# Performance work log

Measured on AMD Instinct MI355X. Metric: run time of the kernel, lower is better.

The kernel has to match this reference:

```python
import jax, jax.numpy as jnp
import numpy as np
from jax import lax

NC = 8  # num_classes
NUM_ITERS = 2


def _resize_bilinear_ac(x, out_h, out_w):
    """Bilinear resize with align_corners=True, x: (N, C, H, W)."""
    N, C, H, W = x.shape

    def coords(n_out, n_in):
        if n_out == 1:
            return jnp.zeros((1,), jnp.float32)
        return jnp.linspace(0.0, float(n_in - 1), n_out, dtype=jnp.float32)

    ys = coords(out_h, H)
    xs = coords(out_w, W)
    y0 = jnp.floor(ys).astype(jnp.int32)
    y1 = jnp.minimum(y0 + 1, H - 1)
    wy = (ys - y0.astype(jnp.float32)).astype(x.dtype)
    x0 = jnp.floor(xs).astype(jnp.int32)
    x1 = jnp.minimum(x0 + 1, W - 1)
    wx = (xs - x0.astype(jnp.float32)).astype(x.dtype)

    r0 = x[:, :, y0, :]
    r1 = x[:, :, y1, :]
    r = r0 * (1.0 - wy)[None, None, :, None] + r1 * wy[None, None, :, None]
    c0 = r[:, :, :, x0]
    c1 = r[:, :, :, x1]
    return c0 * (1.0 - wx)[None, None, None, :] + c1 * wx[None, None, None, :]


def _conv2d(x, w, groups=1):
    k = w.shape[-1]
    pad = k // 2
    return lax.conv_general_dilated(
        x, w, window_strides=(1, 1), padding=[(pad, pad), (pad, pad)],
        dimension_numbers=('NCHW', 'OIHW', 'NCHW'), feature_group_count=groups)


def _mean_field_update(unary, guidance, spatial_w, bilateral_w, compat_w):
    Q = jax.nn.softmax(unary, axis=1)
    cw = compat_w[:, :, 0, 0]  # (O, I)
    for _ in range(NUM_ITERS):
        spatial_msg = _conv2d(Q, spatial_w, groups=NC)          # depthwise 3x3
        bilateral_in = jnp.concatenate([Q, guidance], axis=1)   # (N, NC+6, H, W)
        bilateral_msg = _conv2d(bilateral_in, bilateral_w)      # 3x3 dense
        message = spatial_msg + bilateral_msg
        message = jnp.einsum('nchw,oc->nohw', message, cw)      # 1x1 compat conv
        Q = jax.nn.softmax(unary - message, axis=1)
    return Q


def setup_inputs() -> dict:
    key = jax.random.key(0)
    ks = jax.random.split(key, 16)
    inp = {
        'logits': jax.random.normal(ks[0], (8, NC, 512, 512), jnp.float32),
        'image': jax.random.uniform(ks[1], (8, 3, 512, 512), jnp.float32),
        'skip0': jax.random.normal(ks[2], (8, 64, 256, 256), jnp.float32),
        'skip1': jax.random.normal(ks[3], (8, 128, 128, 128), jnp.float32),
        'skip2': jax.random.normal(ks[4], (8, 256, 64, 64), jnp.float32),
        'skip3': jax.random.normal(ks[5], (8, 512, 32, 32), jnp.float32),
        'spatial_w': jax.random.normal(ks[6], (NC, 1, 3, 3), jnp.float32) * 0.1,
        'bilateral_w': jax.random.normal(ks[7], (NC, NC + 6, 3, 3), jnp.float32) * 0.1,
        # compat_conv is initialized to -I (zeros then -= eye) in the module
        'compat_w': (-jnp.eye(NC, dtype=jnp.float32)).reshape(NC, NC, 1, 1),
        'skip_w0': jax.random.normal(ks[8], (3, 64, 1, 1), jnp.float32) * 0.05,
        'skip_b0': jnp.zeros((3,), jnp.float32),
        'skip_w1': jax.random.normal(ks[9], (3, 128, 1, 1), jnp.float32) * 0.05,
        'skip_b1': jnp.zeros((3,), jnp.float32),
        'skip_w2': jax.random.normal(ks[10], (3, 256, 1, 1), jnp.float32) * 0.05,
        'skip_b2': jnp.zeros((3,), jnp.float32),
        'skip_w3': jax.random.normal(ks[11], (3, 512, 1, 1), jnp.float32) * 0.05,
        'skip_b3': jnp.zeros((3,), jnp.float32),
    }
    return inp


def reference(logits, image, skip0, skip1, skip2, skip3,
              spatial_w, bilateral_w, compat_w,
              skip_w0, skip_b0, skip_w1, skip_b1,
              skip_w2, skip_b2, skip_w3, skip_b3):
    H, W = logits.shape[2], logits.shape[3]

    # fuse_skip_features: 1x1 project each skip to 3ch, upsample, average
    skips = [skip0, skip1, skip2, skip3]
    ws = [skip_w0, skip_w1, skip_w2, skip_w3]
    bs = [skip_b0, skip_b1, skip_b2, skip_b3]
    fused = jnp.zeros((logits.shape[0], 3, H, W), logits.dtype)
    for feat, w, b in zip(skips, ws, bs):
        p = jnp.einsum('nchw,oc->nohw', feat, w[:, :, 0, 0]) + b[None, :, None, None]
        fused = fused + _resize_bilinear_ac(p, H, W)
    fused = fused / len(skips)

    guidance = jnp.concatenate([image, fused], axis=1)  # (N, 6, H, W)

    Q_full = _mean_field_update(logits, guidance, spatial_w, bilateral_w, compat_w)

    logits_down = _resize_bilinear_ac(logits, H // 2, W // 2)
    guidance_down = _resize_bilinear_ac(guidance, H // 2, W // 2)
    Q_down = _mean_field_update(logits_down, guidance_down, spatial_w, bilateral_w, compat_w)
    Q_down_up = _resize_bilinear_ac(Q_down, H, W)

    return (Q_full + Q_down_up) / 2.0
```

## Files before the change

kernel.cpp:

```cpp
#include <hip/hip_runtime.h>
#include <hip/hip_fp16.h>
#include <math.h>

#define NB 8
#define NCLS 8
#define NGU 6
#define NBI 14
#define HF 512
#define WF 512
#define HH 256
#define WH 256

#define TOX 32
#define TOY 16
#define SX 36
#define SY 20
#define SPX (SY * SX)
#define R1W 36
#define R1N (18 * 36)
#define R1T 41
#define R2T 32
#define PLANE (SPX * 8)
#define PSTR (PLANE + 32)
#define TILEH (16 + PSTR + PLANE + 16)

typedef _Float16 f16x8 __attribute__((ext_vector_type(8)));
typedef float f32x4 __attribute__((ext_vector_type(4)));

static __device__ __forceinline__ void ac_prep(int o, float scale, int insz,
                                               int& i0, int& i1, float& f) {
    float s = (float)o * scale;
    int ii = (int)floorf(s);
    if (ii > insz - 1) ii = insz - 1;
    if (ii < 0) ii = 0;
    i0 = ii;
    i1 = (ii + 1 < insz) ? (ii + 1) : (insz - 1);
    f = s - (float)ii;
}

static __device__ __forceinline__ void dma16(const _Float16* g, _Float16* l) {
    __builtin_amdgcn_global_load_lds(
        (const __attribute__((address_space(1))) void*)g,
        (__attribute__((address_space(3))) void*)l, 16, 0, 0);
}

__global__ void k_fill3(float* __restrict__ p1, float* __restrict__ p2,
                        float* __restrict__ p3, const float* __restrict__ b1,
                        const float* __restrict__ b2, const float* __restrict__ b3) {
    int i = blockIdx.x * blockDim.x + threadIdx.x;
    if (i < NB * 3 * 16384) { p1[i] = b1[(i / 16384) % 3]; return; }
    i -= NB * 3 * 16384;
    if (i < NB * 3 * 4096) { p2[i] = b2[(i / 4096) % 3]; return; }
    i -= NB * 3 * 4096;
    if (i < NB * 3 * 1024) p3[i] = b3[(i / 1024) % 3];
}

template <int VEC, bool DIRECT>
__global__ void k_skip_proj(const float* __restrict__ feat, const float* __restrict__ w,
                            const float* __restrict__ bias, float* __restrict__ out,
                            int C, int HW, int nch) {
    __shared__ float sw[3 * 512];
    for (int i = threadIdx.x; i < 3 * C; i += blockDim.x) sw[i] = w[i];
    __syncthreads();
    const int HWv = HW / VEC;
    int total = NB * HWv * nch;
    for (int idx = blockIdx.x * blockDim.x + threadIdx.x; idx < total;
         idx += gridDim.x * blockDim.x) {
        int hv = idx % HWv;
        int t = idx / HWv;
        int ch = t % nch;
        int n = t / nch;
        int c0 = ch * 64;
        const float* fp = feat + ((size_t)n * C + c0) * HW + (size_t)hv * VEC;
        float a[3][VEC];
        #pragma unroll
        for (int o = 0; o < 3; ++o)
            #pragma unroll
            for (int k = 0; k < VEC; ++k) a[o][k] = 0.f;
        #pragma unroll 4
        for (int c = 0; c < 64; ++c) {
            float v[VEC];
            if constexpr (VEC == 4) {
                float4 t4 = *reinterpret_cast<const float4*>(fp + (size_t)c * HW);
                v[0] = t4.x; v[1] = t4.y; v[2] = t4.z; v[3] = t4.w;
            } else if constexpr (VEC == 2) {
                float2 t2 = *reinterpret_cast<const float2*>(fp + (size_t)c * HW);
                v[0] = t2.x; v[1] = t2.y;
            } else {
                v[0] = fp[(size_t)c * HW];
            }
            #pragma unroll
            for (int o = 0; o < 3; ++o) {
                const float wv = sw[o * C + c0 + c];
                #pragma unroll
                for (int k = 0; k < VEC; ++k) a[o][k] = fmaf(wv, v[k], a[o][k]);
            }
        }
        float* op = out + (size_t)n * 3 * HW + (size_t)hv * VEC;
        #pragma unroll
        for (int o = 0; o < 3; ++o) {
            #pragma unroll
            for (int k = 0; k < VEC; ++k) {
                if (DIRECT)
                    op[(size_t)o * HW + k] = bias[o] + a[o][k];
                else
                    atomicAdd(&op[(size_t)o * HW + k], a[o][k]);
            }
        }
    }
}

__global__ void k_prep_full(const float* __restrict__ logits, const float* __restrict__ image,
                            const float* __restrict__ p0, const float* __restrict__ p1,
                            const float* __restrict__ p2, const float* __restrict__ p3,
                            _Float16* __restrict__ Gh, _Float16* __restrict__ Q0h) {
    const int HW = HF * WF;
    int t = blockIdx.x * blockDim.x + threadIdx.x;
    if (t >= NB * HW / 2) return;
    int idx = t * 2;
    int n = idx / HW, r = idx - n * HW;
    int y = r / WF, x = r - y * WF;

    const float* ps[4] = {p0, p1, p2, p3};
    const int ss[4] = {256, 128, 64, 32};
    float f[2][3] = {{0.f, 0.f, 0.f}, {0.f, 0.f, 0.f}};
    #pragma unroll
    for (int l = 0; l < 4; ++l) {
        int s = ss[l];
        float scale = (float)(s - 1) / 511.0f;
        int y0, y1;
        float fy;
        ac_prep(y, scale, s, y0, y1, fy);
        const float* pb = ps[l] + (size_t)n * 3 * s * s;
        #pragma unroll
        for (int k = 0; k < 2; ++k) {
            int x0, x1;
            float fx;
            ac_prep(x + k, scale, s, x0, x1, fx);
            #pragma unroll
            for (int o = 0; o < 3; ++o) {
                const float* pp = pb + (size_t)o * s * s;
                float v00 = pp[y0 * s + x0], v01 = pp[y0 * s + x1];
                float v10 = pp[y1 * s + x0], v11 = pp[y1 * s + x1];
                float r0 = v00 * (1.f - fy) + v10 * fy;
                float r1 = v01 * (1.f - fy) + v11 * fy;
                f[k][o] += r0 * (1.f - fx) + r1 * fx;
            }
        }
    }
    const float* ip = image + (size_t)n * 3 * HW + r;
    float2 img[3];
    #pragma unroll
    for (int o = 0; o < 3; ++o) img[o] = *reinterpret_cast<const float2*>(&ip[(size_t)o * HW]);
    const float* up = logits + (size_t)n * NCLS * HW + r;
    float2 u[8];
    #pragma unroll
    for (int o = 0; o < 8; ++o) u[o] = *reinterpret_cast<const float2*>(&up[(size_t)o * HW]);

    f16x8 gv[2], qv[2];
    #pragma unroll
    for (int k = 0; k < 2; ++k) {
        gv[k][0] = (_Float16)(k ? img[0].y : img[0].x);
        gv[k][1] = (_Float16)(k ? img[1].y : img[1].x);
        gv[k][2] = (_Float16)(k ? img[2].y : img[2].x);
        gv[k][3] = (_Float16)(f[k][0] * 0.25f);
        gv[k][4] = (_Float16)(f[k][1] * 0.25f);
        gv[k][5] = (_Float16)(f[k][2] * 0.25f);
        gv[k][6] = (_Float16)0.f;
        gv[k][7] = (_Float16)0.f;
        float e[8];
        float s = 0.f;
        #pragma unroll
        for (int o = 0; o < 8; ++o) { e[o] = __expf(k ? u[o].y : u[o].x); s += e[o]; }
        float inv = 1.f / s;
        #pragma unroll
        for (int o = 0; o < 8; ++o) qv[k][o] = (_Float16)(e[o] * inv);
    }
    *(f16x8*)(Gh + (size_t)idx * 8) = gv[0];
    *(f16x8*)(Gh + (size_t)idx * 8 + 8) = gv[1];
    *(f16x8*)(Q0h + (size_t)idx * 8) = qv[0];
    *(f16x8*)(Q0h + (size_t)idx * 8 + 8) = qv[1];
}

__global__ void k_prep_wf(const float* __restrict__ wsp, const float* __restrict__ wbil,
                          const float* __restrict__ cw, _Float16* __restrict__ wf) {
    __shared__ float sW2[NBI * 72];
    int tid = threadIdx.x;
    if (tid < NBI * 72) {
        int o = tid & 7;
        int t = (tid >> 3) % 9;
        int ci = tid / 72;
        float s = 0.f;
        for (int c = 0; c < NCLS; ++c)
            s += cw[o * NCLS + c] * wbil[((size_t)c * NBI + ci) * 9 + t];
        if (ci < NCLS) s += cw[o * NCLS + ci] * wsp[ci * 9 + t];
        sW2[tid] = s;
    }
    __syncthreads();
    if (tid < 5 * 64) {
        int l = tid & 63;
        int col = l & 15, kg = l >> 4;
        #pragma unroll
        for (int e = 0; e < 8; ++e) {
            int k = (tid >> 6) * 32 + kg * 8 + e;
            int tap = k >> 4, ci = k & 15;
            float v = (tap < 9 && ci < 14 && col < 8) ? sW2[ci * 72 + tap * 8 + col] : 0.f;
            wf[tid * 8 + e] = (_Float16)v;
        }
    }
}

template <bool DOWN, bool UPFOLD>
__global__ __launch_bounds__(256, 4) void k_mf_mfma(
    const float* __restrict__ unary, const _Float16* __restrict__ Q0h,
    const _Float16* __restrict__ Gh, const _Float16* __restrict__ Qd,
    void* __restrict__ QoutV, const _Float16* __restrict__ wfragG,
    int H, int W, int Hs, int Ws) {
    __shared__ __align__(16) _Float16 s_t[TILEH];
    __shared__ __align__(16) _Float16 s_msg[R1N * 8];
    _Float16* tb0 = s_t + 16;
    _Float16* tb1 = s_t + 16 + PSTR;

    const int tid = threadIdx.x;
    const int lane = tid & 63;
    const int wv = tid >> 6;
    const int n = blockIdx.z;
    const int gx0 = blockIdx.x * TOX;
    const int gy0 = blockIdx.y * TOY;
    const int HW = H * W;
    const int HWs = Hs * Ws;

    f16x8 wf[5];
    #pragma unroll
    for (int j = 0; j < 5; ++j)
        wf[j] = *(const f16x8*)(wfragG + (j * 64 + lane) * 8);

    if (tid < 16) s_t[tid] = (_Float16)0.f;
    else if (tid < 48) s_t[5760 + tid] = (_Float16)0.f;
    else if (tid < 64) s_t[11520 + tid] = (_Float16)0.f;

    const bool interior = !DOWN && gx0 >= 2 && (gx0 + TOX + 2) <= W &&
                          gy0 >= 2 && (gy0 + TOY + 2) <= H;

    if (!DOWN && interior) {
        const size_t nb = (size_t)n * HW;
        for (int c = wv; c < 12; c += 4) {
            int px = c * 64 + lane;
            int yy = px / SX, xx = px - yy * SX;
            size_t goff = (nb + (size_t)(gy0 + yy - 2) * W + (gx0 + xx - 2)) * 8;
            if (px < SPX) {
                dma16(Q0h + goff, tb0 + (size_t)c * 64 * 8);
                dma16(Gh + goff, tb1 + (size_t)c * 64 * 8);
            }
        }
    } else {
        const float syc = DOWN ? (float)(Hs - 1) / (float)(H - 1) : 1.f;
        const float sxc = DOWN ? (float)(Ws - 1) / (float)(W - 1) : 1.f;
        for (int i = tid; i < SPX; i += 256) {
            int yy = i / SX, xx = i - yy * SX;
            int gy = gy0 + yy - 2, gx = gx0 + xx - 2;
            f16x8 qv, gv;
            #pragma unroll
            for (int o = 0; o < 8; ++o) { qv[o] = (_Float16)0.f; gv[o] = (_Float16)0.f; }
            if ((unsigned)gy < (unsigned)H && (unsigned)gx < (unsigned)W) {
                if (DOWN) {
                    int y0, y1, x0, x1;
                    float fy, fx;
                    ac_prep(gy, syc, Hs, y0, y1, fy);
                    ac_prep(gx, sxc, Ws, x0, x1, fx);
                    const float w00 = (1.f - fy) * (1.f - fx), w01 = (1.f - fy) * fx;
                    const float w10 = fy * (1.f - fx), w11 = fy * fx;
                    const size_t o00 = (size_t)y0 * Ws + x0, o01 = (size_t)y0 * Ws + x1;
                    const size_t o10 = (size_t)y1 * Ws + x0, o11 = (size_t)y1 * Ws + x1;
                    const float* ubase = unary + (size_t)n * NCLS * HWs;
                    float e[8];
                    float s = 0.f;
                    #pragma unroll
                    for (int o = 0; o < 8; ++o) {
                        const float* up = ubase + (size_t)o * HWs;
                        float u = w00 * up[o00] + w01 * up[o01] + w10 * up[o10] + w11 * up[o11];
                        e[o] = __expf(u);
                        s += e[o];
                    }
                    float inv = 1.f / s;
                    #pragma unroll
                    for (int o = 0; o < 8; ++o) qv[o] = (_Float16)(e[o] * inv);
                    const size_t gb = (size_t)n * HWs;
                    f16x8 ga = *(const f16x8*)(Gh + (gb + o00) * 8);
                    f16x8 gb2 = *(const f16x8*)(Gh + (gb + o01) * 8);
                    f16x8 gc = *(const f16x8*)(Gh + (gb + o10) * 8);
                    f16x8 gd = *(const f16x8*)(Gh + (gb + o11) * 8);
                    #pragma unroll
                    for (int c = 0; c < 8; ++c) {
                        float g = w00 * (float)ga[c] + w01 * (float)gb2[c] +
                                  w10 * (float)gc[c] + w11 * (float)gd[c];
                        gv[c] = (_Float16)g;
                    }
                } else {
                    const size_t off = ((size_t)n * HW + (size_t)gy * W + gx) * 8;
                    qv = *(const f16x8*)(Q0h + off);
                    gv = *(const f16x8*)(Gh + off);
                }
            }
            *(f16x8*)(tb0 + i * 8) = qv;
            *(f16x8*)(tb1 + i * 8) = gv;
        }
    }
    __syncthreads();

    for (int t = wv; t < R1T; t += 4) {
        int pb = t * 16;
        int p = pb + (lane & 15);
        if (p > R1N - 1) p = R1N - 1;
        int qy = p / R1W;
        int yy = 1 + qy, xx = p - qy * R1W;
        int kg = lane >> 4;
        f32x4 acc = {0.f, 0.f, 0.f, 0.f};
        #pragma unroll
        for (int j = 0; j < 5; ++j) {
            int tap = 2 * j + (kg >> 1);
            if (tap > 8) tap = 8;
            int dy = tap / 3 - 1, dx = tap - (tap / 3) * 3 - 1;
            int idx = (yy + dy) * SX + (xx + dx);
            f16x8 af = *(const f16x8*)(tb0 + (kg & 1) * PSTR + idx * 8);
            acc = __builtin_amdgcn_mfma_f32_16x16x32_f16(af, wf[j], acc, 0, 0, 0);
        }
        int ch = lane & 15;
        if (ch < 8) {
            int pxb = pb + (lane >> 4) * 4;
            #pragma unroll
            for (int r = 0; r < 4; ++r) {
                int px = pxb + r;
                if (px < R1N) s_msg[px * 8 + ch] = (_Float16)acc[r];
            }
        }
    }
    __syncthreads();

    for (int i = tid; i < R1N; i += 256) {
        int qy = i / R1W;
        int yy = 1 + qy, xx = i - qy * R1W;
        int gy = gy0 + yy - 2, gx = gx0 + xx - 2;
        if (interior || ((unsigned)gy < (unsigned)H && (unsigned)gx < (unsigned)W)) {
            f16x8 m = *(const f16x8*)(s_msg + i * 8);
            f16x8 q0 = *(const f16x8*)(tb0 + (i + SX) * 8);
            float e[8];
            float s = 0.f;
            #pragma unroll
            for (int o = 0; o < 8; ++o) {
                e[o] = (float)q0[o] * __expf(-(float)m[o]);
                s += e[o];
            }
            float inv = 1.f / s;
            f16x8 q1;
            #pragma unroll
            for (int o = 0; o < 8; ++o) q1[o] = (_Float16)(e[o] * inv);
            *(f16x8*)(tb0 + (i + SX) * 8) = q1;
        }
    }
    f16x8 m1r[2];
    #pragma unroll
    for (int u2 = 0; u2 < 2; ++u2) {
        int i = tid + 256 * u2;
        int oy = i >> 5, ox = i & 31;
        int r1 = (1 + oy) * R1W + (2 + ox);
        m1r[u2] = *(const f16x8*)(s_msg + r1 * 8);
    }
    __syncthreads();

    for (int t = wv; t < R2T; t += 4) {
        int pb = t * 16;
        int p = pb + (lane & 15);
        int yy = 2 + (p >> 5), xx = 2 + (p & 31);
        int kg = lane >> 4;
        f32x4 acc = {0.f, 0.f, 0.f, 0.f};
        #pragma unroll
        for (int j = 0; j < 5; ++j) {
            int tap = 2 * j + (kg >> 1);
            if (tap > 8) tap = 8;
            int dy = tap / 3 - 1, dx = tap - (tap / 3) * 3 - 1;
            int idx = (yy + dy) * SX + (xx + dx);
            f16x8 af = *(const f16x8*)(tb0 + (kg & 1) * PSTR + idx * 8);
            acc = __builtin_amdgcn_mfma_f32_16x16x32_f16(af, wf[j], acc, 0, 0, 0);
        }
        int ch = lane & 15;
        if (ch < 8) {
            int pxb = pb + (lane >> 4) * 4;
            #pragma unroll
            for (int r = 0; r < 4; ++r) s_msg[(pxb + r) * 8 + ch] = (_Float16)acc[r];
        }
    }
    __syncthreads();

    #pragma unroll
    for (int u2 = 0; u2 < 2; ++u2) {
        int i = tid + 256 * u2;
        int oy = i >> 5, ox = i & 31;
        int gy = gy0 + oy, gx = gx0 + ox;
        f16x8 m2 = *(const f16x8*)(s_msg + i * 8);
        f16x8 q1 = *(const f16x8*)(tb0 + ((2 + oy) * SX + (2 + ox)) * 8);
        float e[8];
        float s = 0.f;
        #pragma unroll
        for (int o = 0; o < 8; ++o) {
            e[o] = (float)q1[o] * __expf((float)m1r[u2][o] - (float)m2[o]);
            s += e[o];
        }
        float inv = 1.f / s;
        if (UPFOLD) {
            float* qp = (float*)QoutV + (size_t)n * NCLS * HW + (size_t)gy * W + gx;
            int y0, y1, x0, x1;
            float fy, fx;
            ac_prep(gy, 255.f / 511.f, HH, y0, y1, fy);
            ac_prep(gx, 255.f / 511.f, WH, x0, x1, fx);
            const float w00 = (1.f - fy) * (1.f - fx), w01 = (1.f - fy) * fx;
            const float w10 = fy * (1.f - fx), w11 = fy * fx;
            const size_t qb = (size_t)n * (HH * WH);
            f16x8 qa = *(const f16x8*)(Qd + (qb + (size_t)y0 * WH + x0) * 8);
            f16x8 qbv = *(const f16x8*)(Qd + (qb + (size_t)y0 * WH + x1) * 8);
            f16x8 qc = *(const f16x8*)(Qd + (qb + (size_t)y1 * WH + x0) * 8);
            f16x8 qdv = *(const f16x8*)(Qd + (qb + (size_t)y1 * WH + x1) * 8);
            #pragma unroll
            for (int o = 0; o < 8; ++o) {
                float v = w00 * (float)qa[o] + w01 * (float)qbv[o] +
                          w10 * (float)qc[o] + w11 * (float)qdv[o];
                qp[(size_t)o * HW] = fmaf(0.5f, e[o] * inv, 0.5f * v);
            }
        } else {
            _Float16* qo = (_Float16*)QoutV + ((size_t)n * HW + (size_t)gy * W + gx) * 8;
            f16x8 q2;
            #pragma unroll
            for (int o = 0; o < 8; ++o) q2[o] = (_Float16)(e[o] * inv);
            *(f16x8*)qo = q2;
        }
    }
}

static inline int cdiv(int a, int b) { return (a + b - 1) / b; }

extern "C" void kernel_launch(void* const* d_in, const int* in_sizes, int n_in,
                              void* d_out, int out_size, void* d_ws, size_t ws_size,
                              hipStream_t stream) {
    const float* logits = (const float*)d_in[0];
    const float* image = (const float*)d_in[1];
    const float* skip0 = (const float*)d_in[2];
    const float* skip1 = (const float*)d_in[3];
    const float* skip2 = (const float*)d_in[4];
    const float* skip3 = (const float*)d_in[5];
    const float* spatial_w = (const float*)d_in[6];
    const float* bilateral_w = (const float*)d_in[7];
    const float* compat_w = (const float*)d_in[8];
    const float* skip_w0 = (const float*)d_in[9];
    const float* skip_b0 = (const float*)d_in[10];
    const float* skip_w1 = (const float*)d_in[11];
    const float* skip_b1 = (const float*)d_in[12];
    const float* skip_w2 = (const float*)d_in[13];
    const float* skip_b2 = (const float*)d_in[14];
    const float* skip_w3 = (const float*)d_in[15];
    const float* skip_b3 = (const float*)d_in[16];
    float* out = (float*)d_out;
    float* ws = (float*)d_ws;

    float* p0 = ws + 0;
    float* p1 = ws + 1572864;
    float* p2 = ws + 1966080;
    float* p3 = ws + 2064384;
    _Float16* wfrag = (_Float16*)(ws + 2110000);
    _Float16* Q0h = (_Float16*)(ws + 4194304);
    _Float16* Gh = (_Float16*)(ws + 12582912);
    _Float16* Qdh = (_Float16*)(ws + 20971520);

    const int HWf = HF * WF;

    k_prep_wf<<<1, 1024, 0, stream>>>(spatial_w, bilateral_w, compat_w, wfrag);

    k_fill3<<<cdiv(NB * 3 * (16384 + 4096 + 1024), 256), 256, 0, stream>>>(
        p1, p2, p3, skip_b1, skip_b2, skip_b3);

    k_skip_proj<4, true><<<cdiv(NB * 16384 * 1, 256), 256, 0, stream>>>(
        skip0, skip_w0, skip_b0, p0, 64, 65536, 1);
    k_skip_proj<4, false><<<cdiv(NB * 4096 * 2, 256), 256, 0, stream>>>(
        skip1, skip_w1, skip_b1, p1, 128, 16384, 2);
    k_skip_proj<2, false><<<cdiv(NB * 2048 * 4, 256), 256, 0, stream>>>(
        skip2, skip_w2, skip_b2, p2, 256, 4096, 4);
    k_skip_proj<1, false><<<cdiv(NB * 1024 * 8, 256), 256, 0, stream>>>(
        skip3, skip_w3, skip_b3, p3, 512, 1024, 8);

    k_prep_full<<<cdiv(NB * HWf / 2, 256), 256, 0, stream>>>(
        logits, image, p0, p1, p2, p3, Gh, Q0h);

    {
        dim3 grid(WH / TOX, HH / TOY, NB);
        k_mf_mfma<true, false><<<grid, 256, 0, stream>>>(
            logits, nullptr, Gh, nullptr, (void*)Qdh, wfrag, HH, WH, HF, WF);
    }

    {
        dim3 grid(WF / TOX, HF / TOY, NB);
        k_mf_mfma<false, true><<<grid, 256, 0, stream>>>(
            nullptr, Q0h, Gh, Qdh, (void*)out, wfrag, HF, WF, HF, WF);
    }
}
```

Before: 226.7 us.

## Merge skip projections into one launch and fold weight prep into bias fill

Merges the bias-fill and fused-weight-preparation kernels into a single k_init launch. It also replaces four per-level skip projection launches with one k_skip_all kernel that dispatches 1024 blocks per level. Each level now gets a different channel split and vector width, giving more channel chunks and more atomics on the coarse levels, so every level fills exactly 262144 threads. The intent is to cut launch count and tail idle time. The cost is more atomic traffic and narrower loads on level 0 (float2 instead of float4).

Result: faster. 195.1 us (-13.9%).

```diff
diff --git a/kernel.cpp b/kernel.cpp
--- a/kernel.cpp
+++ b/kernel.cpp
@@ -44,70 +44,113 @@
         (__attribute__((address_space(3))) void*)l, 16, 0, 0);
 }
 
-__global__ void k_fill3(float* __restrict__ p1, float* __restrict__ p2,
-                        float* __restrict__ p3, const float* __restrict__ b1,
-                        const float* __restrict__ b2, const float* __restrict__ b3) {
-    int i = blockIdx.x * blockDim.x + threadIdx.x;
-    if (i < NB * 3 * 16384) { p1[i] = b1[(i / 16384) % 3]; return; }
-    i -= NB * 3 * 16384;
-    if (i < NB * 3 * 4096) { p2[i] = b2[(i / 4096) % 3]; return; }
-    i -= NB * 3 * 4096;
-    if (i < NB * 3 * 1024) p3[i] = b3[(i / 1024) % 3];
-}
-
-template <int VEC, bool DIRECT>
-__global__ void k_skip_proj(const float* __restrict__ feat, const float* __restrict__ w,
-                            const float* __restrict__ bias, float* __restrict__ out,
-                            int C, int HW, int nch) {
+__global__ __launch_bounds__(256) void k_init(
+    float* __restrict__ p1, float* __restrict__ p2, float* __restrict__ p3,
+    const float* __restrict__ b1, const float* __restrict__ b2, const float* __restrict__ b3,
+    const float* __restrict__ wsp, const float* __restrict__ wbil,
+    const float* __restrict__ cw, _Float16* __restrict__ wf) {
+    int bid = blockIdx.x;
+    int tid = threadIdx.x;
+    if (bid < 2016) {
+        int i = bid * 256 + tid;
+        if (i < NB * 3 * 16384) { p1[i] = b1[(i / 16384) % 3]; return; }
+        i -= NB * 3 * 16384;
+        if (i < NB * 3 * 4096) { p2[i] = b2[(i / 4096) % 3]; return; }
+        i -= NB * 3 * 4096;
+        p3[i] = b3[(i / 1024) % 3];
+        return;
+    }
+    __shared__ float sW2[NBI * 72];
+    for (int i = tid; i < NBI * 72; i += 256) {
+        int o = i & 7;
+        int t = (i >> 3) % 9;
+        int ci = i / 72;
+        float s = 0.f;
+        for (int c = 0; c < NCLS; ++c)
+            s += cw[o * NCLS + c] * wbil[((size_t)c * NBI + ci) * 9 + t];
+        if (ci < NCLS) s += cw[o * NCLS + ci] * wsp[ci * 9 + t];
+        sW2[i] = s;
+    }
+    __syncthreads();
+    for (int i = tid; i < 5 * 64; i += 256) {
+        int l = i & 63;
+        int col = l & 15, kg = l >> 4;
+        #pragma unroll
+        for (int e = 0; e < 8; ++e) {
+            int k = (i >> 6) * 32 + kg * 8 + e;
+            int tap = k >> 4, ci = k & 15;
+            float v = (tap < 9 && ci < 14 && col < 8) ? sW2[ci * 72 + tap * 8 + col] : 0.f;
+            wf[i * 8 + e] = (_Float16)v;
+        }
+    }
+}
+
+template <int VEC, int CH, bool DIRECT>
+static __device__ __forceinline__ void skip_level(
+    const float* __restrict__ feat, const float* __restrict__ sw,
+    const float* __restrict__ bias, float* __restrict__ out,
+    int C, int HW, int nch, int idx) {
+    const int HWv = HW / VEC;
+    int hv = idx % HWv;
+    int t = idx / HWv;
+    int ch = t % nch;
+    int n = t / nch;
+    int c0 = ch * CH;
+    const float* fp = feat + ((size_t)n * C + c0) * HW + (size_t)hv * VEC;
+    float a[3][VEC];
+    #pragma unroll
+    for (int o = 0; o < 3; ++o)
+        #pragma unroll
+        for (int k = 0; k < VEC; ++k) a[o][k] = 0.f;
+    #pragma unroll 8
+    for (int c = 0; c < CH; ++c) {
+        float v[VEC];
+        if constexpr (VEC == 2) {
+            float2 t2 = *reinterpret_cast<const float2*>(fp + (size_t)c * HW);
+            v[0] = t2.x; v[1] = t2.y;
+        } else {
+            v[0] = fp[(size_t)c * HW];
+        }
+        #pragma unroll
+        for (int o = 0; o < 3; ++o) {
+            const float wv = sw[o * C + c0 + c];
+            #pragma unroll
+            for (int k = 0; k < VEC; ++k) a[o][k] = fmaf(wv, v[k], a[o][k]);
+        }
+    }
+    float* op = out + (size_t)n * 3 * HW + (size_t)hv * VEC;
+    #pragma unroll
+    for (int o = 0; o < 3; ++o) {
+        #pragma unroll
+        for (int k = 0; k < VEC; ++k) {
+            if (DIRECT)
+                op[(size_t)o * HW + k] = bias[o] + a[o][k];
+            else
+                atomicAdd(&op[(size_t)o * HW + k], a[o][k]);
+        }
+    }
+}
+
+__global__ __launch_bounds__(256) void k_skip_all(
+    const float* __restrict__ s0, const float* __restrict__ s1,
+    const float* __restrict__ s2, const float* __restrict__ s3,
+    const float* __restrict__ w0, const float* __restrict__ w1,
+    const float* __restrict__ w2, const float* __restrict__ w3,
+    const float* __restrict__ b0,
+    float* __restrict__ p0, float* __restrict__ p1,
+    float* __restrict__ p2, float* __restrict__ p3) {
     __shared__ float sw[3 * 512];
-    for (int i = threadIdx.x; i < 3 * C; i += blockDim.x) sw[i] = w[i];
+    const int bid = blockIdx.x;
+    const int lvl = bid >> 10;
+    const int idx = (bid & 1023) * 256 + threadIdx.x;
+    const float* w = (lvl == 0) ? w0 : (lvl == 1) ? w1 : (lvl == 2) ? w2 : w3;
+    const int C = (lvl == 0) ? 64 : (lvl == 1) ? 128 : (lvl == 2) ? 256 : 512;
+    for (int i = threadIdx.x; i < 3 * C; i += 256) sw[i] = w[i];
     __syncthreads();
-    const int HWv = HW / VEC;
-    int total = NB * HWv * nch;
-    for (int idx = blockIdx.x * blockDim.x + threadIdx.x; idx < total;
-         idx += gridDim.x * blockDim.x) {
-        int hv = idx % HWv;
-        int t = idx / HWv;
-        int ch = t % nch;
-        int n = t / nch;
-        int c0 = ch * 64;
-        const float* fp = feat + ((size_t)n * C + c0) * HW + (size_t)hv * VEC;
-        float a[3][VEC];
-        #pragma unroll
-        for (int o = 0; o < 3; ++o)
-            #pragma unroll
-            for (int k = 0; k < VEC; ++k) a[o][k] = 0.f;
-        #pragma unroll 4
-        for (int c = 0; c < 64; ++c) {
-            float v[VEC];
-            if constexpr (VEC == 4) {
-                float4 t4 = *reinterpret_cast<const float4*>(fp + (size_t)c * HW);
-                v[0] = t4.x; v[1] = t4.y; v[2] = t4.z; v[3] = t4.w;
-            } else if constexpr (VEC == 2) {
-                float2 t2 = *reinterpret_cast<const float2*>(fp + (size_t)c * HW);
-                v[0] = t2.x; v[1] = t2.y;
-            } else {
-                v[0] = fp[(size_t)c * HW];
-            }
-            #pragma unroll
-            for (int o = 0; o < 3; ++o) {
-                const float wv = sw[o * C + c0 + c];
-                #pragma unroll
-                for (int k = 0; k < VEC; ++k) a[o][k] = fmaf(wv, v[k], a[o][k]);
-            }
-        }
-        float* op = out + (size_t)n * 3 * HW + (size_t)hv * VEC;
-        #pragma unroll
-        for (int o = 0; o < 3; ++o) {
-            #pragma unroll
-            for (int k = 0; k < VEC; ++k) {
-                if (DIRECT)
-                    op[(size_t)o * HW + k] = bias[o] + a[o][k];
-                else
-                    atomicAdd(&op[(size_t)o * HW + k], a[o][k]);
-            }
-        }
-    }
+    if (lvl == 0)      skip_level<2, 64, true >(s0, sw, b0, p0, 64, 65536, 1, idx);
+    else if (lvl == 1) skip_level<2, 32, false>(s1, sw, nullptr, p1, 128, 16384, 4, idx);
+    else if (lvl == 2) skip_level<1, 32, false>(s2, sw, nullptr, p2, 256, 4096, 8, idx);
+    else               skip_level<1, 16, false>(s3, sw, nullptr, p3, 512, 1024, 32, idx);
 }
 
 __global__ void k_prep_full(const float* __restrict__ logits, const float* __restrict__ image,
@@ -180,34 +223,6 @@
     *(f16x8*)(Gh + (size_t)idx * 8 + 8) = gv[1];
     *(f16x8*)(Q0h + (size_t)idx * 8) = qv[0];
     *(f16x8*)(Q0h + (size_t)idx * 8 + 8) = qv[1];
-}
-
-__global__ void k_prep_wf(const float* __restrict__ wsp, const float* __restrict__ wbil,
-                          const float* __restrict__ cw, _Float16* __restrict__ wf) {
-    __shared__ float sW2[NBI * 72];
-    int tid = threadIdx.x;
-    if (tid < NBI * 72) {
-        int o = tid & 7;
-        int t = (tid >> 3) % 9;
-        int ci = tid / 72;
-        float s = 0.f;
-        for (int c = 0; c < NCLS; ++c)
-            s += cw[o * NCLS + c] * wbil[((size_t)c * NBI + ci) * 9 + t];
-        if (ci < NCLS) s += cw[o * NCLS + ci] * wsp[ci * 9 + t];
-        sW2[tid] = s;
-    }
-    __syncthreads();
-    if (tid < 5 * 64) {
-        int l = tid & 63;
-        int col = l & 15, kg = l >> 4;
-        #pragma unroll
-        for (int e = 0; e < 8; ++e) {
-            int k = (tid >> 6) * 32 + kg * 8 + e;
-            int tap = k >> 4, ci = k & 15;
-            float v = (tap < 9 && ci < 14 && col < 8) ? sW2[ci * 72 + tap * 8 + col] : 0.f;
-            wf[tid * 8 + e] = (_Float16)v;
-        }
-    }
 }
 
 template <bool DOWN, bool UPFOLD>
@@ -472,19 +487,12 @@
 
     const int HWf = HF * WF;
 
-    k_prep_wf<<<1, 1024, 0, stream>>>(spatial_w, bilateral_w, compat_w, wfrag);
-
-    k_fill3<<<cdiv(NB * 3 * (16384 + 4096 + 1024), 256), 256, 0, stream>>>(
-        p1, p2, p3, skip_b1, skip_b2, skip_b3);
-
-    k_skip_proj<4, true><<<cdiv(NB * 16384 * 1, 256), 256, 0, stream>>>(
-        skip0, skip_w0, skip_b0, p0, 64, 65536, 1);
-    k_skip_proj<4, false><<<cdiv(NB * 4096 * 2, 256), 256, 0, stream>>>(
-        skip1, skip_w1, skip_b1, p1, 128, 16384, 2);
-    k_skip_proj<2, false><<<cdiv(NB * 2048 * 4, 256), 256, 0, stream>>>(
-        skip2, skip_w2, skip_b2, p2, 256, 4096, 4);
-    k_skip_proj<1, false><<<cdiv(NB * 1024 * 8, 256), 256, 0, stream>>>(
-        skip3, skip_w3, skip_b3, p3, 512, 1024, 8);
+    k_init<<<2017, 256, 0, stream>>>(p1, p2, p3, skip_b1, skip_b2, skip_b3,
+                                     spatial_w, bilateral_w, compat_w, wfrag);
+
+    k_skip_all<<<4096, 256, 0, stream>>>(skip0, skip1, skip2, skip3,
+                                         skip_w0, skip_w1, skip_w2, skip_w3,
+                                         skip_b0, p0, p1, p2, p3);
 
     k_prep_full<<<cdiv(NB * HWf / 2, 256), 256, 0, stream>>>(
         logits, image, p0, p1, p2, p3, Gh, Q0h);
```

## Fuse skip projections into one kernel with LDS-staged DMA loads

Applied to the files above, without the earlier changes.

Replaces the bias fill kernel and four per-level skip projection launches with a single k_skip_all kernel. Block ranges are assigned to each pyramid level, and each block streams 64-channel slabs of 256 pixels into shared memory via global_load_lds, then reduces all channels itself. This removes the atomicAdd split-channel accumulation and the separate bias fill, and cuts five launches to one. In exchange each block needs 64KB of LDS, which limits occupancy, and it synchronizes twice per channel group.

Result: faster. 200.2 us (-11.7%).

```diff
diff --git a/kernel.cpp b/kernel.cpp
--- a/kernel.cpp
+++ b/kernel.cpp
@@ -43,143 +43,10 @@
         (const __attribute__((address_space(1))) void*)g,
         (__attribute__((address_space(3))) void*)l, 16, 0, 0);
 }
-
-__global__ void k_fill3(float* __restrict__ p1, float* __restrict__ p2,
-                        float* __restrict__ p3, const float* __restrict__ b1,
-                        const float* __restrict__ b2, const float* __restrict__ b3) {
-    int i = blockIdx.x * blockDim.x + threadIdx.x;
-    if (i < NB * 3 * 16384) { p1[i] = b1[(i / 16384) % 3]; return; }
-    i -= NB * 3 * 16384;
-    if (i < NB * 3 * 4096) { p2[i] = b2[(i / 4096) % 3]; return; }
-    i -= NB * 3 * 4096;
-    if (i < NB * 3 * 1024) p3[i] = b3[(i / 1024) % 3];
-}
-
-template <int VEC, bool DIRECT>
-__global__ void k_skip_proj(const float* __restrict__ feat, const float* __restrict__ w,
-                            const float* __restrict__ bias, float* __restrict__ out,
-                            int C, int HW, int nch) {
-    __shared__ float sw[3 * 512];
-    for (int i = threadIdx.x; i < 3 * C; i += blockDim.x) sw[i] = w[i];
-    __syncthreads();
-    const int HWv = HW / VEC;
-    int total = NB * HWv * nch;
-    for (int idx = blockIdx.x * blockDim.x + threadIdx.x; idx < total;
-         idx += gridDim.x * blockDim.x) {
-        int hv = idx % HWv;
-        int t = idx / HWv;
-        int ch = t % nch;
-        int n = t / nch;
-        int c0 = ch * 64;
-        const float* fp = feat + ((size_t)n * C + c0) * HW + (size_t)hv * VEC;
-        float a[3][VEC];
-        #pragma unroll
-        for (int o = 0; o < 3; ++o)
-            #pragma unroll
-            for (int k = 0; k < VEC; ++k) a[o][k] = 0.f;
-        #pragma unroll 4
-        for (int c = 0; c < 64; ++c) {
-            float v[VEC];
-            if constexpr (VEC == 4) {
-                float4 t4 = *reinterpret_cast<const float4*>(fp + (size_t)c * HW);
-                v[0] = t4.x; v[1] = t4.y; v[2] = t4.z; v[3] = t4.w;
-            } else if constexpr (VEC == 2) {
-                float2 t2 = *reinterpret_cast<const float2*>(fp + (size_t)c * HW);
-                v[0] = t2.x; v[1] = t2.y;
-            } else {
-                v[0] = fp[(size_t)c * HW];
-            }
-            #pragma unroll
-            for (int o = 0; o < 3; ++o) {
-                const float wv = sw[o * C + c0 + c];
-                #pragma unroll
-                for (int k = 0; k < VEC; ++k) a[o][k] = fmaf(wv, v[k], a[o][k]);
-            }
-        }
-        float* op = out + (size_t)n * 3 * HW + (size_t)hv * VEC;
-        #pragma unroll
-        for (int o = 0; o < 3; ++o) {
-            #pragma unroll
-            for (int k = 0; k < VEC; ++k) {
-                if (DIRECT)
-                    op[(size_t)o * HW + k] = bias[o] + a[o][k];
-                else
-                    atomicAdd(&op[(size_t)o * HW + k], a[o][k]);
-            }
-        }
-    }
-}
-
-__global__ void k_prep_full(const float* __restrict__ logits, const float* __restrict__ image,
-                            const float* __restrict__ p0, const float* __restrict__ p1,
-                            const float* __restrict__ p2, const float* __restrict__ p3,
-                            _Float16* __restrict__ Gh, _Float16* __restrict__ Q0h) {
-    const int HW = HF * WF;
-    int t = blockIdx.x * blockDim.x + threadIdx.x;
-    if (t >= NB * HW / 2) return;
-    int idx = t * 2;
-    int n = idx / HW, r = idx - n * HW;
-    int y = r / WF, x = r - y * WF;
-
-    const float* ps[4] = {p0, p1, p2, p3};
-    const int ss[4] = {256, 128, 64, 32};
-    float f[2][3] = {{0.f, 0.f, 0.f}, {0.f, 0.f, 0.f}};
-    #pragma unroll
-    for (int l = 0; l < 4; ++l) {
-        int s = ss[l];
-        float scale = (float)(s - 1) / 511.0f;
-        int y0, y1;
-        float fy;
-        ac_prep(y, scale, s, y0, y1, fy);
-        const float* pb = ps[l] + (size_t)n * 3 * s * s;
-        #pragma unroll
-        for (int k = 0; k < 2; ++k) {
-            int x0, x1;
-            float fx;
-            ac_prep(x + k, scale, s, x0, x1, fx);
-            #pragma unroll
-            for (int o = 0; o < 3; ++o) {
-                const float* pp = pb + (size_t)o * s * s;
-                float v00 = pp[y0 * s + x0], v01 = pp[y0 * s + x1];
-                float v10 = pp[y1 * s + x0], v11 = pp[y1 * s + x1];
-                float r0 = v00 * (1.f - fy) + v10 * fy;
-                float r1 = v01 * (1.f - fy) + v11 * fy;
-                f[k][o] += r0 * (1.f - fx) + r1 * fx;
-            }
-        }
-    }
-    const float* ip = image + (size_t)n * 3 * HW + r;
-    float2 img[3];
-    #pragma unroll
-    for (int o = 0; o < 3; ++o) img[o] = *reinterpret_cast<const float2*>(&ip[(size_t)o * HW]);
-    const float* up = logits + (size_t)n * NCLS * HW + r;
-    float2 u[8];
-    #pragma unroll
-    for (int o = 0; o < 8; ++o) u[o] = *reinterpret_cast<const float2*>(&up[(size_t)o * HW]);
-
-    f16x8 gv[2], qv[2];
-    #pragma unroll
-    for (int k = 0; k < 2; ++k) {
-        gv[k][0] = (_Float16)(k ? img[0].y : img[0].x);
-        gv[k][1] = (_Float16)(k ? img[1].y : img[1].x);
-        gv[k][2] = (_Float16)(k ? img[2].y : img[2].x);
-        gv[k][3] = (_Float16)(f[k][0] * 0.25f);
-        gv[k][4] = (_Float16)(f[k][1] * 0.25f);
-        gv[k][5] = (_Float16)(f[k][2] * 0.25f);
-        gv[k][6] = (_Float16)0.f;
-        gv[k][7] = (_Float16)0.f;
-        float e[8];
-        float s = 0.f;
-        #pragma unroll
-        for (int o = 0; o < 8; ++o) { e[o] = __expf(k ? u[o].y : u[o].x); s += e[o]; }
-        float inv = 1.f / s;
-        #pragma unroll
-        for (int o = 0; o < 8; ++o) qv[k][o] = (_Float16)(e[o] * inv);
-    }
-    *(f16x8*)(Gh + (size_t)idx * 8) = gv[0];
-    *(f16x8*)(Gh + (size_t)idx * 8 + 8) = gv[1];
-    *(f16x8*)(Q0h + (size_t)idx * 8) = qv[0];
-    *(f16x8*)(Q0h + (size_t)idx * 8 + 8) = qv[1];
+static __device__ __forceinline__ void dma16f(const float* g, float* l) {
+    __builtin_amdgcn_global_load_lds(
+        (const __attribute__((address_space(1))) void*)g,
+        (__attribute__((address_space(3))) void*)l, 16, 0, 0);
 }
 
 __global__ void k_prep_wf(const float* __restrict__ wsp, const float* __restrict__ wbil,
@@ -208,6 +75,133 @@
             wf[tid * 8 + e] = (_Float16)v;
         }
     }
+}
+
+template <int C, int HW>
+static __device__ __forceinline__ void skip_run(
+    const float* __restrict__ feat, const float* __restrict__ wg,
+    const float* __restrict__ bg, float* __restrict__ out, int idx,
+    float* st, float* sw, int tid, int lane, int wv) {
+    for (int i = tid; i < 3 * C; i += 256) sw[i] = wg[i];
+    const int pxg = idx * 256;
+    const int n = pxg / HW;
+    const int hw0 = pxg - n * HW;
+    const float* fb = feat + (size_t)n * C * HW + hw0;
+    float a0 = 0.f, a1 = 0.f, a2 = 0.f;
+    for (int g = 0; g < C; g += 64) {
+        for (int r = wv; r < 64; r += 4)
+            dma16f(fb + (size_t)(g + r) * HW + lane * 4, st + r * 256);
+        __syncthreads();
+        #pragma unroll
+        for (int c = 0; c < 64; ++c) {
+            const float v = st[c * 256 + tid];
+            a0 = fmaf(sw[g + c], v, a0);
+            a1 = fmaf(sw[C + g + c], v, a1);
+            a2 = fmaf(sw[2 * C + g + c], v, a2);
+        }
+        __syncthreads();
+    }
+    float* op = out + (size_t)n * 3 * HW + hw0 + tid;
+    op[0] = bg[0] + a0;
+    op[HW] = bg[1] + a1;
+    op[2 * (size_t)HW] = bg[2] + a2;
+}
+
+__global__ __launch_bounds__(256) void k_skip_all(
+    const float* __restrict__ s0, const float* __restrict__ s1,
+    const float* __restrict__ s2, const float* __restrict__ s3,
+    const float* __restrict__ w0, const float* __restrict__ w1,
+    const float* __restrict__ w2, const float* __restrict__ w3,
+    const float* __restrict__ b0, const float* __restrict__ b1,
+    const float* __restrict__ b2, const float* __restrict__ b3,
+    float* __restrict__ p0, float* __restrict__ p1,
+    float* __restrict__ p2, float* __restrict__ p3) {
+    __shared__ __align__(16) float st[64 * 256];
+    __shared__ float sw[3 * 512];
+    const int bid = blockIdx.x;
+    const int tid = threadIdx.x;
+    const int lane = tid & 63;
+    const int wv = tid >> 6;
+    if (bid < 32)
+        skip_run<512, 1024>(s3, w3, b3, p3, bid, st, sw, tid, lane, wv);
+    else if (bid < 160)
+        skip_run<256, 4096>(s2, w2, b2, p2, bid - 32, st, sw, tid, lane, wv);
+    else if (bid < 672)
+        skip_run<128, 16384>(s1, w1, b1, p1, bid - 160, st, sw, tid, lane, wv);
+    else
+        skip_run<64, 65536>(s0, w0, b0, p0, bid - 672, st, sw, tid, lane, wv);
+}
+
+__global__ void k_prep_full(const float* __restrict__ logits, const float* __restrict__ image,
+                            const float* __restrict__ p0, const float* __restrict__ p1,
+                            const float* __restrict__ p2, const float* __restrict__ p3,
+                            _Float16* __restrict__ Gh, _Float16* __restrict__ Q0h) {
+    const int HW = HF * WF;
+    int t = blockIdx.x * blockDim.x + threadIdx.x;
+    if (t >= NB * HW / 2) return;
+    int idx = t * 2;
+    int n = idx / HW, r = idx - n * HW;
+    int y = r / WF, x = r - y * WF;
+
+    const float* ps[4] = {p0, p1, p2, p3};
+    const int ss[4] = {256, 128, 64, 32};
+    float f[2][3] = {{0.f, 0.f, 0.f}, {0.f, 0.f, 0.f}};
+    #pragma unroll
+    for (int l = 0; l < 4; ++l) {
+        int s = ss[l];
+        float scale = (float)(s - 1) / 511.0f;
+        int y0, y1;
+        float fy;
+        ac_prep(y, scale, s, y0, y1, fy);
+        const float* pb = ps[l] + (size_t)n * 3 * s * s;
+        #pragma unroll
+        for (int k = 0; k < 2; ++k) {
+            int x0, x1;
+            float fx;
+            ac_prep(x + k, scale, s, x0, x1, fx);
+            #pragma unroll
+            for (int o = 0; o < 3; ++o) {
+                const float* pp = pb + (size_t)o * s * s;
+                float v00 = pp[y0 * s + x0], v01 = pp[y0 * s + x1];
+                float v10 = pp[y1 * s + x0], v11 = pp[y1 * s + x1];
+                float r0 = v00 * (1.f - fy) + v10 * fy;
+                float r1 = v01 * (1.f - fy) + v11 * fy;
+                f[k][o] += r0 * (1.f - fx) + r1 * fx;
+            }
+        }
+    }
+    const float* ip = image + (size_t)n * 3 * HW + r;
+    float2 img[3];
+    #pragma unroll
+    for (int o = 0; o < 3; ++o) img[o] = *reinterpret_cast<const float2*>(&ip[(size_t)o * HW]);
+    const float* up = logits + (size_t)n * NCLS * HW + r;
+    float2 u[8];
+    #pragma unroll
+    for (int o = 0; o < 8; ++o) u[o] = *reinterpret_cast<const float2*>(&up[(size_t)o * HW]);
+
+    f16x8 gv[2], qv[2];
+    #pragma unroll
+    for (int k = 0; k < 2; ++k) {
+        gv[k][0] = (_Float16)(k ? img[0].y : img[0].x);
+        gv[k][1] = (_Float16)(k ? img[1].y : img[1].x);
+        gv[k][2] = (_Float16)(k ? img[2].y : img[2].x);
+        gv[k][3] = (_Float16)(f[k][0] * 0.25f);
+        gv[k][4] = (_Float16)(f[k][1] * 0.25f);
+        gv[k][5] = (_Float16)(f[k][2] * 0.25f);
+        gv[k][6] = (_Float16)0.f;
+        gv[k][7] = (_Float16)0.f;
+        float e[8];
+        float s = 0.f;
+        #pragma unroll
+        for (int o = 0; o < 8; ++o) { e[o] = __expf(k ? u[o].y : u[o].x); s += e[o]; }
+        float inv = 1.f / s;
+        #pragma unroll
+        for (int o = 0; o < 8; ++o) qv[k][o] = (_Float16)(e[o] * inv);
+    }
+    *(f16x8*)(Gh + (size_t)idx * 8) = gv[0];
+    *(f16x8*)(Gh + (size_t)idx * 8 + 8) = gv[1];
+    *(f16x8*)(Q0h + (size_t)idx * 8) = qv[0];
+    *(f16x8*)(Q0h + (size_t)idx * 8 + 8) = qv[1];
 }
 
 template <bool DOWN, bool UPFOLD>
@@ -474,17 +468,10 @@
 
     k_prep_wf<<<1, 1024, 0, stream>>>(spatial_w, bilateral_w, compat_w, wfrag);
 
-    k_fill3<<<cdiv(NB * 3 * (16384 + 4096 + 1024), 256), 256, 0, stream>>>(
-        p1, p2, p3, skip_b1, skip_b2, skip_b3);
-
-    k_skip_proj<4, true><<<cdiv(NB * 16384 * 1, 256), 256, 0, stream>>>(
-        skip0, skip_w0, skip_b0, p0, 64, 65536, 1);
-    k_skip_proj<4, false><<<cdiv(NB * 4096 * 2, 256), 256, 0, stream>>>(
-        skip1, skip_w1, skip_b1, p1, 128, 16384, 2);
-    k_skip_proj<2, false><<<cdiv(NB * 2048 * 4, 256), 256, 0, stream>>>(
-        skip2, skip_w2, skip_b2, p2, 256, 4096, 4);
-    k_skip_proj<1, false><<<cdiv(NB * 1024 * 8, 256), 256, 0, stream>>>(
-        skip3, skip_w3, skip_b3, p3, 512, 1024, 8);
+    k_skip_all<<<2720, 256, 0, stream>>>(skip0, skip1, skip2, skip3,
+                                         skip_w0, skip_w1, skip_w2, skip_w3,
+                                         skip_b0, skip_b1, skip_b2, skip_b3,
+                                         p0, p1, p2, p3);
 
     k_prep_full<<<cdiv(NB * HWf / 2, 256), 256, 0, stream>>>(
         logits, image, p0, p1, p2, p3, Gh, Q0h);
```
